# Performance work log

Measured on AMD Instinct MI355X. Metric: run time of the kernel, lower is better.

The kernel has to match this reference:

```python
import jax, jax.numpy as jnp
import numpy as np

T, E, H, D = 4, 1024, 16, 128  # batch, seq, heads, per-head dim (== embed_dim)
C = H * D                      # attention_concat_dim


def setup_inputs() -> dict:
    rng = jax.random.key(0)
    ks = jax.random.split(rng, 16)
    def lin_w(k, fan_in, fan_out):
        bound = 1.0 / np.sqrt(fan_in)
        return jax.random.uniform(k, (fan_out, fan_in), jnp.float32, -bound, bound)
    def lin_b(k, fan_in, fan_out):
        bound = 1.0 / np.sqrt(fan_in)
        return jax.random.uniform(k, (fan_out,), jnp.float32, -bound, bound)
    return {
        "key":   jax.random.normal(ks[0], (T, E, D), jnp.float32),
        "value": jax.random.normal(ks[1], (T, E, D), jnp.float32),
        "query": jax.random.normal(ks[2], (T, E, D), jnp.float32),
        "Wq": lin_w(ks[3], D, C), "bq": lin_b(ks[4], D, C),
        "Wk": lin_w(ks[5], D, C), "bk": lin_b(ks[6], D, C),
        "Wv": lin_w(ks[7], D, C), "bv": lin_b(ks[8], D, C),
        "Wo": lin_w(ks[9], C, D), "bo": lin_b(ks[10], C, D),
    }


def reference(key, value, query, Wq, bq, Wk, bk, Wv, bv, Wo, bo):
    # QKV projections (embed_dim -> n_heads*embed_dim), then split heads
    q = (query @ Wq.T + bq).reshape(T, E, H, D)
    k = (key   @ Wk.T + bk).reshape(T, E, H, D)
    v = (value @ Wv.T + bv).reshape(T, E, H, D)
    # memory-efficient attention math == standard scaled dot-product attention
    q = q * (1.0 / np.sqrt(D))
    scores = jnp.einsum("tqhd,tkhd->thqk", q, k)  # [T,H,E,E]
    causal = jnp.tril(jnp.ones((E, E), dtype=bool))  # _init_causal_mask(E, E)
    scores = jnp.where(causal[None, None, :, :], scores, jnp.finfo(scores.dtype).min)
    probs = jax.nn.softmax(scores, axis=-1)
    attended = jnp.einsum("thqk,tkhd->tqhd", probs, v).reshape(T, E, C)
    # dropout_p = 0.0 (eval) -> identity; output projection
    return attended @ Wo.T + bo
```

## Files before the change

kernel.cpp:

```cpp
#include <hip/hip_runtime.h>

#define T_ 4
#define E_ 1024
#define H_ 16
#define D_ 128
#define C_ 2048
#define QK_SCALE 0.08838834764831845f
#define LOG2E 1.4426950408889634f

typedef short s16x8 __attribute__((ext_vector_type(8)));
typedef float f32x4 __attribute__((ext_vector_type(4)));

__device__ __forceinline__ unsigned short f2bf(float x) {
    unsigned u = __builtin_bit_cast(unsigned, x);
    u = (u + 0x7FFFu + ((u >> 16) & 1u)) >> 16;
    return (unsigned short)u;
}

__device__ __forceinline__ unsigned cvt_pk(float lo, float hi) {
    unsigned r;
    asm("v_cvt_pk_bf16_f32 %0, %1, %2" : "=v"(r) : "v"(lo), "v"(hi));
    return r;
}

#define MFMA16(a, b, c) __builtin_amdgcn_mfma_f32_16x16x32_bf16((a), (b), (c), 0, 0, 0)

__device__ __forceinline__ void gload_lds16(const unsigned short* g, unsigned short* l) {
    __builtin_amdgcn_global_load_lds(
        (const __attribute__((address_space(1))) unsigned int*)g,
        (__attribute__((address_space(3))) unsigned int*)l, 16, 0, 0);
}

__global__ __launch_bounds__(256) void cvt7_kernel(
    const float* __restrict__ q, const float* __restrict__ k, const float* __restrict__ v,
    const float* __restrict__ wq, const float* __restrict__ wk, const float* __restrict__ wv,
    const float* __restrict__ wo,
    unsigned short* __restrict__ base, unsigned short* __restrict__ wo16)
{
    const int b = blockIdx.x;
    const float* src;
    unsigned short* dst;
    int lb;
    if (b < 256)       { src = q;  dst = base;            lb = b; }
    else if (b < 512)  { src = k;  dst = base + 524288;   lb = b - 256; }
    else if (b < 768)  { src = v;  dst = base + 1048576;  lb = b - 512; }
    else if (b < 896)  { src = wq; dst = base + 1572864;  lb = b - 768; }
    else if (b < 1024) { src = wk; dst = base + 1835008;  lb = b - 896; }
    else if (b < 1152) { src = wv; dst = base + 2097152;  lb = b - 1024; }
    else               { src = wo; dst = wo16;            lb = b - 1152; }
    const int i = (lb * 256 + threadIdx.x) * 8;
    float4 a = *reinterpret_cast<const float4*>(src + i);
    float4 c = *reinterpret_cast<const float4*>(src + i + 4);
    s16x8 r;
    r[0] = (short)f2bf(a.x); r[1] = (short)f2bf(a.y);
    r[2] = (short)f2bf(a.z); r[3] = (short)f2bf(a.w);
    r[4] = (short)f2bf(c.x); r[5] = (short)f2bf(c.y);
    r[6] = (short)f2bf(c.z); r[7] = (short)f2bf(c.w);
    *reinterpret_cast<s16x8*>(dst + i) = r;
}

__global__ __launch_bounds__(256) void qkv_kernel(
    const unsigned short* __restrict__ Xq, const unsigned short* __restrict__ Xk,
    const unsigned short* __restrict__ Xv,
    const unsigned short* __restrict__ Wq_, const unsigned short* __restrict__ Wk_,
    const unsigned short* __restrict__ Wv_,
    const float* __restrict__ bq_, const float* __restrict__ bk_, const float* __restrict__ bv_,
    unsigned short* __restrict__ oq, unsigned short* __restrict__ okk,
    unsigned short* __restrict__ ov)
{
    __shared__ unsigned short S[2][128 * 128];

    const int z = blockIdx.z;
    const unsigned short* X = (z == 0) ? Xq : (z == 1) ? Xk : Xv;
    const unsigned short* W = (z == 0) ? Wq_ : (z == 1) ? Wk_ : Wv_;
    const float* Bv = (z == 0) ? bq_ : (z == 1) ? bk_ : bv_;
    unsigned short* out = (z == 0) ? oq : (z == 1) ? okk : ov;
    const float scale = (z == 0) ? (QK_SCALE * LOG2E) : 1.0f;

    const int tid = threadIdx.x;
    const int w = tid >> 6;
    const int lane = tid & 63;
    const int lr = lane & 15;
    const int lg = lane >> 4;
    const int nbase = blockIdx.y * 128;
    const size_t xrow0 = (size_t)blockIdx.x * 128;

#pragma unroll
    for (int it = 0; it < 8; ++it) {
        const int f = it * 256 + tid;
        const int kk = f >> 4;
        const int cs = ((f & 15) * 8) ^ ((kk & 7) << 3);
        gload_lds16(&X[(xrow0 + kk) * D_ + cs], &S[0][f * 8]);
        gload_lds16(&W[(size_t)(nbase + kk) * D_ + cs], &S[1][f * 8]);
    }
    __syncthreads();

    const int key = (lr & 7) << 3;
    s16x8 af[2][4];
#pragma unroll
    for (int mi = 0; mi < 2; ++mi)
#pragma unroll
        for (int kc = 0; kc < 4; ++kc)
            af[mi][kc] = *reinterpret_cast<const s16x8*>(
                &S[0][(w * 32 + mi * 16 + lr) * 128 + ((kc * 32 + lg * 8) ^ key)]);

    f32x4 acc[2][8];
#pragma unroll
    for (int mi = 0; mi < 2; ++mi)
#pragma unroll
        for (int n = 0; n < 8; ++n) acc[mi][n] = f32x4{0.f, 0.f, 0.f, 0.f};

#pragma unroll
    for (int n = 0; n < 8; ++n) {
        s16x8 bf[4];
#pragma unroll
        for (int kc = 0; kc < 4; ++kc)
            bf[kc] = *reinterpret_cast<const s16x8*>(
                &S[1][(n * 16 + lr) * 128 + ((kc * 32 + lg * 8) ^ key)]);
#pragma unroll
        for (int mi = 0; mi < 2; ++mi)
#pragma unroll
            for (int kc = 0; kc < 4; ++kc)
                acc[mi][n] = MFMA16(af[mi][kc], bf[kc], acc[mi][n]);
    }

    float bias[8];
#pragma unroll
    for (int n = 0; n < 8; ++n) bias[n] = Bv[nbase + n * 16 + lr];

    __syncthreads();
    unsigned short* Tile = &S[0][0];

    if (z < 2) {
#pragma unroll
        for (int mi = 0; mi < 2; ++mi)
#pragma unroll
            for (int i = 0; i < 4; ++i) {
                const int rowl = w * 32 + mi * 16 + lg * 4 + i;
                float v0 = (acc[mi][0][i] + bias[0]) * scale;
                float v1 = (acc[mi][1][i] + bias[1]) * scale;
                float v2 = (acc[mi][2][i] + bias[2]) * scale;
                float v3 = (acc[mi][3][i] + bias[3]) * scale;
                float v4 = (acc[mi][4][i] + bias[4]) * scale;
                float v5 = (acc[mi][5][i] + bias[5]) * scale;
                float v6 = (acc[mi][6][i] + bias[6]) * scale;
                float v7 = (acc[mi][7][i] + bias[7]) * scale;
                union { s16x8 s; unsigned u[4]; } pk;
                pk.u[0] = cvt_pk(v0, v1);
                pk.u[1] = cvt_pk(v2, v3);
                pk.u[2] = cvt_pk(v4, v5);
                pk.u[3] = cvt_pk(v6, v7);
                *reinterpret_cast<s16x8*>(&Tile[rowl * 136 + 8 * lr]) = pk.s;
            }
    } else {
#pragma unroll
        for (int n = 0; n < 8; ++n) {
            union { s16x8 s; unsigned u[4]; } pk;
            pk.u[0] = cvt_pk(acc[0][n][0] + bias[n], acc[0][n][1] + bias[n]);
            pk.u[1] = cvt_pk(acc[0][n][2] + bias[n], acc[0][n][3] + bias[n]);
            pk.u[2] = cvt_pk(acc[1][n][0] + bias[n], acc[1][n][1] + bias[n]);
            pk.u[3] = cvt_pk(acc[1][n][2] + bias[n], acc[1][n][3] + bias[n]);
            *reinterpret_cast<s16x8*>(&Tile[(n * 16 + lr) * 136 + w * 32 + 8 * lg]) = pk.s;
        }
    }
    __syncthreads();

    const int t = (blockIdx.x * 128) >> 10;
    const int e0 = (blockIdx.x * 128) & 1023;
    const int hh = blockIdx.y;
    const int row16 = tid >> 4;
    const int c8 = (tid & 15) * 8;
    if (z < 2) {
        unsigned short* dst = out + (((size_t)(t * H_ + hh) * E_ + e0) * D_);
#pragma unroll
        for (int j = 0; j < 8; ++j) {
            const int row = j * 16 + row16;
            *reinterpret_cast<s16x8*>(dst + (size_t)row * D_ + c8) =
                *reinterpret_cast<const s16x8*>(&Tile[row * 136 + c8]);
        }
    } else {
        unsigned short* dst = out + ((size_t)(t * H_ + hh) * D_) * E_ + e0;
#pragma unroll
        for (int j = 0; j < 8; ++j) {
            const int row = j * 16 + row16;
            *reinterpret_cast<s16x8*>(dst + (size_t)row * E_ + c8) =
                *reinterpret_cast<const s16x8*>(&Tile[row * 136 + c8]);
        }
    }
}

__global__ __launch_bounds__(512, 4) void attn_kernel(
    const unsigned short* __restrict__ Q, const unsigned short* __restrict__ K,
    const unsigned short* __restrict__ Vt, unsigned short* __restrict__ O)
{
    __shared__ unsigned short K_lds[2][64 * 128];
    __shared__ unsigned short Vt_lds[2][128 * 64];

    const int tid = threadIdx.x;
    const int w = tid >> 6;
    const int lane = tid & 63;
    const int lr = lane & 15;
    const int g = lane >> 4;
    const int th = blockIdx.x;
    const int t = th >> 4;
    const int h = th & 15;
    const int p = blockIdx.y;
    const int qblk = (p < 4) ? (7 - p) : (p - 4);
    const int q0w = qblk * 128 + w * 16;
    const int nkv = 2 * qblk + 2;

    const unsigned short* Qh = Q + th * (E_ * D_);
    const unsigned short* Kh = K + th * (E_ * D_);
    const unsigned short* Vth = Vt + th * (D_ * E_);

    const int fA = tid, fB = 512 + tid;
    const unsigned short* gkA = Kh + (fA >> 4) * D_ + (((fA & 15) * 8) ^ (((fA >> 4) & 7) << 3));
    const unsigned short* gkB = Kh + (fB >> 4) * D_ + (((fB & 15) * 8) ^ (((fB >> 4) & 7) << 3));
    const unsigned short* gvA = Vth + (fA >> 3) * E_ + (((fA & 7) * 8) ^ (((fA >> 3) & 7) << 3));
    const unsigned short* gvB = Vth + (fB >> 3) * E_ + (((fB & 7) * 8) ^ (((fB >> 3) & 7) << 3));

    s16x8 qb[4];
#pragma unroll
    for (int kc = 0; kc < 4; ++kc)
        qb[kc] = *reinterpret_cast<const s16x8*>(
            &Qh[(q0w + lr) * D_ + kc * 32 + g * 8]);

    s16x8 ones;
#pragma unroll
    for (int j = 0; j < 8; ++j) ones[j] = (short)0x3F80;

    f32x4 ot[8];
    f32x4 lac;
    float m = -1e30f;
#pragma unroll
    for (int dt = 0; dt < 8; ++dt) ot[dt] = f32x4{0.f, 0.f, 0.f, 0.f};
    lac = f32x4{0.f, 0.f, 0.f, 0.f};

    gload_lds16(gkA, &K_lds[0][fA * 8]);
    gload_lds16(gkB, &K_lds[0][fB * 8]);
    gload_lds16(gvA, &Vt_lds[0][fA * 8]);
    gload_lds16(gvB, &Vt_lds[0][fB * 8]);
    gkA += 64 * D_; gkB += 64 * D_; gvA += 64; gvB += 64;

    int cur = 0;
    for (int kb = 0; kb < nkv; ++kb) {
        const int kv0 = kb * 64;
        __syncthreads();

        if (kb + 1 < nkv) {
            gload_lds16(gkA, &K_lds[cur ^ 1][fA * 8]);
            gload_lds16(gkB, &K_lds[cur ^ 1][fB * 8]);
            gload_lds16(gvA, &Vt_lds[cur ^ 1][fA * 8]);
            gload_lds16(gvB, &Vt_lds[cur ^ 1][fB * 8]);
            gkA += 64 * D_; gkB += 64 * D_; gvA += 64; gvB += 64;
        }

        if (kv0 <= q0w + 15) {
            const unsigned short* Kb = K_lds[cur];
            const unsigned short* Vb = Vt_lds[cur];
            const int key = (lr & 7) << 3;

            f32x4 st[4];
            __builtin_amdgcn_s_setprio(1);
#pragma unroll
            for (int kvi = 0; kvi < 4; ++kvi) {
                s16x8 kf[4];
#pragma unroll
                for (int kc = 0; kc < 4; ++kc)
                    kf[kc] = *reinterpret_cast<const s16x8*>(
                        &Kb[(kvi * 16 + lr) * 128 + ((kc * 32 + g * 8) ^ key)]);
                f32x4 a = f32x4{0.f, 0.f, 0.f, 0.f};
#pragma unroll
                for (int kc = 0; kc < 4; ++kc) a = MFMA16(kf[kc], qb[kc], a);
                st[kvi] = a;
            }
            __builtin_amdgcn_s_setprio(0);

            if (kv0 + 63 > q0w) {
                const int q = q0w + lr;
#pragma unroll
                for (int kvi = 0; kvi < 4; ++kvi)
#pragma unroll
                    for (int i = 0; i < 4; ++i) {
                        const int kv = kv0 + kvi * 16 + g * 4 + i;
                        if (kv > q) st[kvi][i] = -1e30f;
                    }
            }

            float a0 = fmaxf(fmaxf(st[0][0], st[0][1]), fmaxf(st[0][2], st[0][3]));
            float a1 = fmaxf(fmaxf(st[1][0], st[1][1]), fmaxf(st[1][2], st[1][3]));
            float a2 = fmaxf(fmaxf(st[2][0], st[2][1]), fmaxf(st[2][2], st[2][3]));
            float a3 = fmaxf(fmaxf(st[3][0], st[3][1]), fmaxf(st[3][2], st[3][3]));
            float pm = fmaxf(fmaxf(a0, a1), fmaxf(a2, a3));
            pm = fmaxf(pm, __shfl_xor(pm, 16));
            pm = fmaxf(pm, __shfl_xor(pm, 32));

            if (__any(pm > m + 8.f)) {
                const float mn = fmaxf(m, pm);
                const float esc = exp2f(m - mn);
                m = mn;
                lac *= esc;
#pragma unroll
                for (int dt = 0; dt < 8; ++dt) ot[dt] *= esc;
            }

            s16x8 pb[2];
#pragma unroll
            for (int kc = 0; kc < 2; ++kc) {
                float e0 = exp2f(st[2 * kc][0] - m);
                float e1 = exp2f(st[2 * kc][1] - m);
                float e2 = exp2f(st[2 * kc][2] - m);
                float e3 = exp2f(st[2 * kc][3] - m);
                float f0 = exp2f(st[2 * kc + 1][0] - m);
                float f1 = exp2f(st[2 * kc + 1][1] - m);
                float f2 = exp2f(st[2 * kc + 1][2] - m);
                float f3 = exp2f(st[2 * kc + 1][3] - m);
                union { s16x8 s; unsigned u[4]; } pk;
                pk.u[0] = cvt_pk(e0, e1);
                pk.u[1] = cvt_pk(e2, e3);
                pk.u[2] = cvt_pk(f0, f1);
                pk.u[3] = cvt_pk(f2, f3);
                pb[kc] = pk.s;
            }

            lac = MFMA16(ones, pb[0], lac);
            lac = MFMA16(ones, pb[1], lac);

            __builtin_amdgcn_s_setprio(1);
#pragma unroll
            for (int dt = 0; dt < 8; ++dt) {
                const int rb = (dt * 16 + lr) * 64;
#pragma unroll
                for (int kc = 0; kc < 2; ++kc) {
                    s16x8 va = *reinterpret_cast<const s16x8*>(
                        &Vb[rb + ((kc * 32 + 8 * g) ^ key)]);
                    ot[dt] = MFMA16(va, pb[kc], ot[dt]);
                }
            }
            __builtin_amdgcn_s_setprio(0);
        }
        cur ^= 1;
    }

    unsigned short* Ob = O + (size_t)t * E_ * C_ + h * D_;
    const float rl = 1.0f / lac[0];
    const int q = q0w + lr;
#pragma unroll
    for (int dt = 0; dt < 8; ++dt) {
        uint2 val;
        val.x = cvt_pk(ot[dt][0] * rl, ot[dt][1] * rl);
        val.y = cvt_pk(ot[dt][2] * rl, ot[dt][3] * rl);
        *reinterpret_cast<uint2*>(&Ob[(size_t)q * C_ + dt * 16 + 4 * g]) = val;
    }
}

__global__ __launch_bounds__(256) void oproj_partial(
    const unsigned short* __restrict__ A, const unsigned short* __restrict__ Wo16,
    float* __restrict__ part)
{
    const int tid = threadIdx.x;
    const int w = tid >> 6;
    const int lane = tid & 63;
    const int lr = lane & 15;
    const int lg = lane >> 4;
    const int mbase = blockIdx.x * 16;
    const int ncol = w * 32;
    const int k0 = blockIdx.y * 512;
    float* myp = part + (size_t)blockIdx.y * (4096 * 128);

    f32x4 acc0 = f32x4{0.f, 0.f, 0.f, 0.f};
    f32x4 acc1 = f32x4{0.f, 0.f, 0.f, 0.f};
    const unsigned short* Arow = A + (size_t)(mbase + lr) * C_ + k0;
    const unsigned short* W0 = Wo16 + (size_t)(ncol + lr) * C_ + k0;
    const unsigned short* W1 = Wo16 + (size_t)(ncol + 16 + lr) * C_ + k0;

#pragma unroll 8
    for (int kb = 0; kb < 16; ++kb) {
        const int ko = kb * 32 + lg * 8;
        s16x8 af = *reinterpret_cast<const s16x8*>(Arow + ko);
        s16x8 b0 = *reinterpret_cast<const s16x8*>(W0 + ko);
        s16x8 b1 = *reinterpret_cast<const s16x8*>(W1 + ko);
        acc0 = MFMA16(af, b0, acc0);
        acc1 = MFMA16(af, b1, acc1);
    }

#pragma unroll
    for (int n = 0; n < 2; ++n) {
        const f32x4 acc = n ? acc1 : acc0;
        const int col = ncol + n * 16 + lr;
#pragma unroll
        for (int i = 0; i < 4; ++i)
            myp[(mbase + lg * 4 + i) * D_ + col] = acc[i];
    }
}

__global__ __launch_bounds__(256) void oproj_reduce(
    const float* __restrict__ part, const float* __restrict__ bo,
    float* __restrict__ out)
{
    const int iv = blockIdx.x * 256 + threadIdx.x;
    const size_t seg = (size_t)4096 * 128;
    float4 s = *reinterpret_cast<const float4*>(part + (size_t)iv * 4);
#pragma unroll
    for (int y = 1; y < 4; ++y) {
        float4 v = *reinterpret_cast<const float4*>(part + y * seg + (size_t)iv * 4);
        s.x += v.x; s.y += v.y; s.z += v.z; s.w += v.w;
    }
    const float4 b = *reinterpret_cast<const float4*>(bo + ((iv & 31) * 4));
    s.x += b.x; s.y += b.y; s.z += b.z; s.w += b.w;
    *reinterpret_cast<float4*>(out + (size_t)iv * 4) = s;
}

extern "C" void kernel_launch(void* const* d_in, const int* in_sizes, int n_in,
                              void* d_out, int out_size, void* d_ws, size_t ws_size,
                              hipStream_t stream) {
    const float* key   = (const float*)d_in[0];
    const float* value = (const float*)d_in[1];
    const float* query = (const float*)d_in[2];
    const float* Wq = (const float*)d_in[3];
    const float* bq = (const float*)d_in[4];
    const float* Wk = (const float*)d_in[5];
    const float* bk = (const float*)d_in[6];
    const float* Wv = (const float*)d_in[7];
    const float* bv = (const float*)d_in[8];
    const float* Wo = (const float*)d_in[9];
    const float* bo = (const float*)d_in[10];
    float* out = (float*)d_out;

    unsigned short* ws = (unsigned short*)d_ws;
    const size_t QKV_ELEMS = (size_t)T_ * H_ * E_ * D_;
    unsigned short* q_ws = ws;
    unsigned short* k_ws = ws + QKV_ELEMS;
    unsigned short* v_ws = ws + 2 * QKV_ELEMS;
    unsigned short* att_ws = ws + 3 * QKV_ELEMS;
    unsigned short* wo16_ws = ws + 4 * QKV_ELEMS;
    float* part_ws = (float*)k_ws;

    unsigned short* xq16 = att_ws;
    unsigned short* xk16 = att_ws + 524288;
    unsigned short* xv16 = att_ws + 1048576;
    unsigned short* wq16 = att_ws + 1572864;
    unsigned short* wk16 = att_ws + 1835008;
    unsigned short* wv16 = att_ws + 2097152;

    cvt7_kernel<<<dim3(1280), 256, 0, stream>>>(query, key, value, Wq, Wk, Wv, Wo,
                                                att_ws, wo16_ws);
    qkv_kernel<<<dim3(32, 16, 3), 256, 0, stream>>>(xq16, xk16, xv16,
                                                    wq16, wk16, wv16,
                                                    bq, bk, bv,
                                                    q_ws, k_ws, v_ws);
    attn_kernel<<<dim3(64, 8), 512, 0, stream>>>(q_ws, k_ws, v_ws, att_ws);
    oproj_partial<<<dim3(256, 4), 256, 0, stream>>>(att_ws, wo16_ws, part_ws);
    oproj_reduce<<<dim3(512), 256, 0, stream>>>(part_ws, bo, out);
}
```

Measured before the change: 89.97 us.

## Pair complementary causal query blocks per workgroup to share K/V tiles

Each attention workgroup now handles two query blocks, a late block (7-p) and an early block (p), so every block does the same total causal work. The K/V tiles already loaded into LDS are reused for both blocks' QK and PV MFMAs. The grid is halved to 64x4 and the launch bound drops to 2 waves per SIMD to make room for the doubled accumulators. The intent is to cut redundant K/V loads and balance work across blocks, at the cost of higher register pressure and fewer resident workgroups.

```diff
diff --git a/kernel.cpp b/kernel.cpp
--- a/kernel.cpp
+++ b/kernel.cpp
@@ -189,7 +189,7 @@
     }
 }
 
-__global__ __launch_bounds__(512, 4) void attn_kernel(
+__global__ __launch_bounds__(512, 2) void attn_kernel(
     const unsigned short* __restrict__ Q, const unsigned short* __restrict__ K,
     const unsigned short* __restrict__ Vt, unsigned short* __restrict__ O)
 {
@@ -205,9 +205,11 @@
     const int t = th >> 4;
     const int h = th & 15;
     const int p = blockIdx.y;
-    const int qblk = (p < 4) ? (7 - p) : (p - 4);
-    const int q0w = qblk * 128 + w * 16;
-    const int nkv = 2 * qblk + 2;
+    const int qA = 7 - p;
+    const int qB = p;
+    const int q0A = qA * 128 + w * 16;
+    const int q0B = qB * 128 + w * 16;
+    const int nkv = 2 * qA + 2;
 
     const unsigned short* Qh = Q + th * (E_ * D_);
     const unsigned short* Kh = K + th * (E_ * D_);
@@ -219,22 +221,27 @@
     const unsigned short* gvA = Vth + (fA >> 3) * E_ + (((fA & 7) * 8) ^ (((fA >> 3) & 7) << 3));
     const unsigned short* gvB = Vth + (fB >> 3) * E_ + (((fB & 7) * 8) ^ (((fB >> 3) & 7) << 3));
 
-    s16x8 qb[4];
-#pragma unroll
-    for (int kc = 0; kc < 4; ++kc)
-        qb[kc] = *reinterpret_cast<const s16x8*>(
-            &Qh[(q0w + lr) * D_ + kc * 32 + g * 8]);
+    s16x8 qbA[4], qbB[4];
+#pragma unroll
+    for (int kc = 0; kc < 4; ++kc) {
+        qbA[kc] = *reinterpret_cast<const s16x8*>(&Qh[(q0A + lr) * D_ + kc * 32 + g * 8]);
+        qbB[kc] = *reinterpret_cast<const s16x8*>(&Qh[(q0B + lr) * D_ + kc * 32 + g * 8]);
+    }
 
     s16x8 ones;
 #pragma unroll
     for (int j = 0; j < 8; ++j) ones[j] = (short)0x3F80;
 
-    f32x4 ot[8];
-    f32x4 lac;
-    float m = -1e30f;
-#pragma unroll
-    for (int dt = 0; dt < 8; ++dt) ot[dt] = f32x4{0.f, 0.f, 0.f, 0.f};
-    lac = f32x4{0.f, 0.f, 0.f, 0.f};
+    f32x4 otA[8], otB[8];
+    f32x4 lacA, lacB;
+    float mA = -1e30f, mB = -1e30f;
+#pragma unroll
+    for (int dt = 0; dt < 8; ++dt) {
+        otA[dt] = f32x4{0.f, 0.f, 0.f, 0.f};
+        otB[dt] = f32x4{0.f, 0.f, 0.f, 0.f};
+    }
+    lacA = f32x4{0.f, 0.f, 0.f, 0.f};
+    lacB = f32x4{0.f, 0.f, 0.f, 0.f};
 
     gload_lds16(gkA, &K_lds[0][fA * 8]);
     gload_lds16(gkB, &K_lds[0][fB * 8]);
@@ -255,12 +262,13 @@
             gkA += 64 * D_; gkB += 64 * D_; gvA += 64; gvB += 64;
         }
 
-        if (kv0 <= q0w + 15) {
+        if (kv0 <= q0A + 15) {
+            const bool doB = (kv0 <= q0B + 15);
             const unsigned short* Kb = K_lds[cur];
             const unsigned short* Vb = Vt_lds[cur];
             const int key = (lr & 7) << 3;
 
-            f32x4 st[4];
+            f32x4 stA[4], stB[4];
             __builtin_amdgcn_s_setprio(1);
 #pragma unroll
             for (int kvi = 0; kvi < 4; ++kvi) {
@@ -271,71 +279,138 @@
                         &Kb[(kvi * 16 + lr) * 128 + ((kc * 32 + g * 8) ^ key)]);
                 f32x4 a = f32x4{0.f, 0.f, 0.f, 0.f};
 #pragma unroll
-                for (int kc = 0; kc < 4; ++kc) a = MFMA16(kf[kc], qb[kc], a);
-                st[kvi] = a;
+                for (int kc = 0; kc < 4; ++kc) a = MFMA16(kf[kc], qbA[kc], a);
+                stA[kvi] = a;
+                if (doB) {
+                    f32x4 b = f32x4{0.f, 0.f, 0.f, 0.f};
+#pragma unroll
+                    for (int kc = 0; kc < 4; ++kc) b = MFMA16(kf[kc], qbB[kc], b);
+                    stB[kvi] = b;
+                }
             }
             __builtin_amdgcn_s_setprio(0);
 
-            if (kv0 + 63 > q0w) {
-                const int q = q0w + lr;
+            if (kv0 + 63 > q0A) {
+                const int q = q0A + lr;
 #pragma unroll
                 for (int kvi = 0; kvi < 4; ++kvi)
 #pragma unroll
                     for (int i = 0; i < 4; ++i) {
                         const int kv = kv0 + kvi * 16 + g * 4 + i;
-                        if (kv > q) st[kvi][i] = -1e30f;
+                        if (kv > q) stA[kvi][i] = -1e30f;
                     }
             }
-
-            float a0 = fmaxf(fmaxf(st[0][0], st[0][1]), fmaxf(st[0][2], st[0][3]));
-            float a1 = fmaxf(fmaxf(st[1][0], st[1][1]), fmaxf(st[1][2], st[1][3]));
-            float a2 = fmaxf(fmaxf(st[2][0], st[2][1]), fmaxf(st[2][2], st[2][3]));
-            float a3 = fmaxf(fmaxf(st[3][0], st[3][1]), fmaxf(st[3][2], st[3][3]));
-            float pm = fmaxf(fmaxf(a0, a1), fmaxf(a2, a3));
-            pm = fmaxf(pm, __shfl_xor(pm, 16));
-            pm = fmaxf(pm, __shfl_xor(pm, 32));
-
-            if (__any(pm > m + 8.f)) {
-                const float mn = fmaxf(m, pm);
-                const float esc = exp2f(m - mn);
-                m = mn;
-                lac *= esc;
-#pragma unroll
-                for (int dt = 0; dt < 8; ++dt) ot[dt] *= esc;
-            }
-
-            s16x8 pb[2];
+            if (doB && (kv0 + 63 > q0B)) {
+                const int q = q0B + lr;
+#pragma unroll
+                for (int kvi = 0; kvi < 4; ++kvi)
+#pragma unroll
+                    for (int i = 0; i < 4; ++i) {
+                        const int kv = kv0 + kvi * 16 + g * 4 + i;
+                        if (kv > q) stB[kvi][i] = -1e30f;
+                    }
+            }
+
+            {
+                float a0 = fmaxf(fmaxf(stA[0][0], stA[0][1]), fmaxf(stA[0][2], stA[0][3]));
+                float a1 = fmaxf(fmaxf(stA[1][0], stA[1][1]), fmaxf(stA[1][2], stA[1][3]));
+                float a2 = fmaxf(fmaxf(stA[2][0], stA[2][1]), fmaxf(stA[2][2], stA[2][3]));
+                float a3 = fmaxf(fmaxf(stA[3][0], stA[3][1]), fmaxf(stA[3][2], stA[3][3]));
+                float pm = fmaxf(fmaxf(a0, a1), fmaxf(a2, a3));
+                pm = fmaxf(pm, __shfl_xor(pm, 16));
+                pm = fmaxf(pm, __shfl_xor(pm, 32));
+                if (__any(pm > mA + 8.f)) {
+                    const float mn = fmaxf(mA, pm);
+                    const float esc = exp2f(mA - mn);
+                    mA = mn;
+                    lacA *= esc;
+#pragma unroll
+                    for (int dt = 0; dt < 8; ++dt) otA[dt] *= esc;
+                }
+            }
+            s16x8 pbA[2];
 #pragma unroll
             for (int kc = 0; kc < 2; ++kc) {
-                float e0 = exp2f(st[2 * kc][0] - m);
-                float e1 = exp2f(st[2 * kc][1] - m);
-                float e2 = exp2f(st[2 * kc][2] - m);
-                float e3 = exp2f(st[2 * kc][3] - m);
-                float f0 = exp2f(st[2 * kc + 1][0] - m);
-                float f1 = exp2f(st[2 * kc + 1][1] - m);
-                float f2 = exp2f(st[2 * kc + 1][2] - m);
-                float f3 = exp2f(st[2 * kc + 1][3] - m);
+                float e0 = exp2f(stA[2 * kc][0] - mA);
+                float e1 = exp2f(stA[2 * kc][1] - mA);
+                float e2 = exp2f(stA[2 * kc][2] - mA);
+                float e3 = exp2f(stA[2 * kc][3] - mA);
+                float f0 = exp2f(stA[2 * kc + 1][0] - mA);
+                float f1 = exp2f(stA[2 * kc + 1][1] - mA);
+                float f2 = exp2f(stA[2 * kc + 1][2] - mA);
+                float f3 = exp2f(stA[2 * kc + 1][3] - mA);
                 union { s16x8 s; unsigned u[4]; } pk;
                 pk.u[0] = cvt_pk(e0, e1);
                 pk.u[1] = cvt_pk(e2, e3);
                 pk.u[2] = cvt_pk(f0, f1);
                 pk.u[3] = cvt_pk(f2, f3);
-                pb[kc] = pk.s;
-            }
-
-            lac = MFMA16(ones, pb[0], lac);
-            lac = MFMA16(ones, pb[1], lac);
+                pbA[kc] = pk.s;
+            }
+            lacA = MFMA16(ones, pbA[0], lacA);
+            lacA = MFMA16(ones, pbA[1], lacA);
+
+            s16x8 pbB[2];
+            if (doB) {
+                float a0 = fmaxf(fmaxf(stB[0][0], stB[0][1]), fmaxf(stB[0][2], stB[0][3]));
+                float a1 = fmaxf(fmaxf(stB[1][0], stB[1][1]), fmaxf(stB[1][2], stB[1][3]));
+                float a2 = fmaxf(fmaxf(stB[2][0], stB[2][1]), fmaxf(stB[2][2], stB[2][3]));
+                float a3 = fmaxf(fmaxf(stB[3][0], stB[3][1]), fmaxf(stB[3][2], stB[3][3]));
+                float pm = fmaxf(fmaxf(a0, a1), fmaxf(a2, a3));
+                pm = fmaxf(pm, __shfl_xor(pm, 16));
+                pm = fmaxf(pm, __shfl_xor(pm, 32));
+                if (__any(pm > mB + 8.f)) {
+                    const float mn = fmaxf(mB, pm);
+                    const float esc = exp2f(mB - mn);
+                    mB = mn;
+                    lacB *= esc;
+#pragma unroll
+                    for (int dt = 0; dt < 8; ++dt) otB[dt] *= esc;
+                }
+#pragma unroll
+                for (int kc = 0; kc < 2; ++kc) {
+                    float e0 = exp2f(stB[2 * kc][0] - mB);
+                    float e1 = exp2f(stB[2 * kc][1] - mB);
+                    float e2 = exp2f(stB[2 * kc][2] - mB);
+                    float e3 = exp2f(stB[2 * kc][3] - mB);
+                    float f0 = exp2f(stB[2 * kc + 1][0] - mB);
+                    float f1 = exp2f(stB[2 * kc + 1][1] - mB);
+                    float f2 = exp2f(stB[2 * kc + 1][2] - mB);
+                    float f3 = exp2f(stB[2 * kc + 1][3] - mB);
+                    union { s16x8 s; unsigned u[4]; } pk;
+                    pk.u[0] = cvt_pk(e0, e1);
+                    pk.u[1] = cvt_pk(e2, e3);
+                    pk.u[2] = cvt_pk(f0, f1);
+                    pk.u[3] = cvt_pk(f2, f3);
+                    pbB[kc] = pk.s;
+                }
+                lacB = MFMA16(ones, pbB[0], lacB);
+                lacB = MFMA16(ones, pbB[1], lacB);
+            }
 
             __builtin_amdgcn_s_setprio(1);
-#pragma unroll
-            for (int dt = 0; dt < 8; ++dt) {
-                const int rb = (dt * 16 + lr) * 64;
-#pragma unroll
-                for (int kc = 0; kc < 2; ++kc) {
-                    s16x8 va = *reinterpret_cast<const s16x8*>(
-                        &Vb[rb + ((kc * 32 + 8 * g) ^ key)]);
-                    ot[dt] = MFMA16(va, pb[kc], ot[dt]);
+            if (doB) {
+#pragma unroll
+                for (int dt = 0; dt < 8; ++dt) {
+                    const int rb = (dt * 16 + lr) * 64;
+#pragma unroll
+                    for (int kc = 0; kc < 2; ++kc) {
+                        s16x8 va = *reinterpret_cast<const s16x8*>(
+                            &Vb[rb + ((kc * 32 + 8 * g) ^ key)]);
+                        otA[dt] = MFMA16(va, pbA[kc], otA[dt]);
+                        otB[dt] = MFMA16(va, pbB[kc], otB[dt]);
+                    }
                 }
+            } else {
+#pragma unroll
+                for (int dt = 0; dt < 8; ++dt) {
+                    const int rb = (dt * 16 + lr) * 64;
+#pragma unroll
+                    for (int kc = 0; kc < 2; ++kc) {
+                        s16x8 va = *reinterpret_cast<const s16x8*>(
+                            &Vb[rb + ((kc * 32 + 8 * g) ^ key)]);
+                        otA[dt] = MFMA16(va, pbA[kc], otA[dt]);
+                    }
+                }
             }
             __builtin_amdgcn_s_setprio(0);
         }
@@ -343,14 +418,27 @@
     }
 
     unsigned short* Ob = O + (size_t)t * E_ * C_ + h * D_;
-    const float rl = 1.0f / lac[0];
-    const int q = q0w + lr;
-#pragma unroll
-    for (int dt = 0; dt < 8; ++dt) {
-        uint2 val;
-        val.x = cvt_pk(ot[dt][0] * rl, ot[dt][1] * rl);
-        val.y = cvt_pk(ot[dt][2] * rl, ot[dt][3] * rl);
-        *reinterpret_cast<uint2*>(&Ob[(size_t)q * C_ + dt * 16 + 4 * g]) = val;
+    {
+        const float rl = 1.0f / lacA[0];
+        const int q = q0A + lr;
+#pragma unroll
+        for (int dt = 0; dt < 8; ++dt) {
+            uint2 val;
+            val.x = cvt_pk(otA[dt][0] * rl, otA[dt][1] * rl);
+            val.y = cvt_pk(otA[dt][2] * rl, otA[dt][3] * rl);
+            *reinterpret_cast<uint2*>(&Ob[(size_t)q * C_ + dt * 16 + 4 * g]) = val;
+        }
+    }
+    {
+        const float rl = 1.0f / lacB[0];
+        const int q = q0B + lr;
+#pragma unroll
+        for (int dt = 0; dt < 8; ++dt) {
+            uint2 val;
+            val.x = cvt_pk(otB[dt][0] * rl, otB[dt][1] * rl);
+            val.y = cvt_pk(otB[dt][2] * rl, otB[dt][3] * rl);
+            *reinterpret_cast<uint2*>(&Ob[(size_t)q * C_ + dt * 16 + 4 * g]) = val;
+        }
     }
 }
 
@@ -449,7 +537,7 @@
                                                     wq16, wk16, wv16,
                                                     bq, bk, bv,
                                                     q_ws, k_ws, v_ws);
-    attn_kernel<<<dim3(64, 8), 512, 0, stream>>>(q_ws, k_ws, v_ws, att_ws);
+    attn_kernel<<<dim3(64, 4), 512, 0, stream>>>(q_ws, k_ws, v_ws, att_ws);
     oproj_partial<<<dim3(256, 4), 256, 0, stream>>>(att_ws, wo16_ws, part_ws);
     oproj_reduce<<<dim3(512), 256, 0, stream>>>(part_ws, bo, out);
 }
```

New measurement: 95.08 us. 1.06x slower.
